# Performance work log

Hardware: AMD Instinct MI355X
Metric: run time of the kernel (lower is better)

The kernel has to match this reference:

```python
import jax, jax.numpy as jnp
import numpy as np

N = 50000   # nodes
E = 600000  # edges (avg degree 12)
D = 128     # embedding_dim == hidden_features
L = 4       # depth


def setup_inputs() -> dict:
    key = jax.random.key(0)
    k0, k1, k2, k3 = jax.random.split(key, 4)
    scale = 1.0 / np.sqrt(D)
    node_embedding = jax.random.normal(k0, (N, D), jnp.float32)
    edge_index = jax.random.randint(k1, (2, E), 0, N, dtype=jnp.int32)
    Ws_rel = jax.random.normal(k2, (L, D, D), jnp.float32) * scale
    bs_rel = jnp.zeros((L, D), jnp.float32)
    Ws_root = jax.random.normal(k3, (L, D, D), jnp.float32) * scale
    return {
        'node_embedding': node_embedding,
        'edge_index': edge_index,
        'Ws_rel': Ws_rel,
        'bs_rel': bs_rel,
        'Ws_root': Ws_root,
    }


def reference(node_embedding, edge_index, Ws_rel, bs_rel, Ws_root):
    # PyG GraphConv (aggr='mean'), flow source_to_target:
    #   out_i = lin_rel(mean_{j in N(i)} x_j) + lin_root(x_i)
    # followed by ELU (dropout probs are 0 -> identity).
    n = node_embedding.shape[0]
    src, dst = edge_index[0], edge_index[1]
    ones = jnp.ones((edge_index.shape[1],), node_embedding.dtype)
    deg = jax.ops.segment_sum(ones, dst, num_segments=n)
    inv_deg = (1.0 / jnp.maximum(deg, 1.0))[:, None]  # [n, 1]
    X = node_embedding
    for l in range(Ws_rel.shape[0]):
        agg = jax.ops.segment_sum(X[src], dst, num_segments=n) * inv_deg  # [n, D]
        out = agg @ Ws_rel[l] + bs_rel[l] + X @ Ws_root[l]
        X = jax.nn.elu(out)
    return X
```

## Files before the change

kernel.cpp:

```cpp
#include <hip/hip_runtime.h>

#define D 128
#define LDR 264
#define SLOTS 64
#define EPB 2048

typedef short bf16x8 __attribute__((ext_vector_type(8)));
typedef float f32x4 __attribute__((ext_vector_type(4)));

__device__ __forceinline__ unsigned short f2bf(float f) {
  unsigned int u = __float_as_uint(f);
  unsigned int r = (u + 0x7fff + ((u >> 16) & 1)) >> 16;
  return (unsigned short)r;
}
__device__ __forceinline__ unsigned int pack2bf(float lo, float hi) {
  return (unsigned int)f2bf(lo) | ((unsigned int)f2bf(hi) << 16);
}

__global__ __launch_bounds__(256) void k_build(
    const int* __restrict__ src, const int* __restrict__ dst, int E, int N,
    int* __restrict__ cursor, unsigned short* __restrict__ csr64,
    const float* __restrict__ X0, unsigned short* __restrict__ Xb, int total4,
    const float* __restrict__ Wrel, const float* __restrict__ Wroot,
    unsigned short* __restrict__ Wp, int wtot,
    int fb, int cb) {
  int b = blockIdx.x;
  if (b < fb) {
    int p = b & 7;
    int chunk = b >> 3;
    int lo = (int)((long long)p * N / 8);
    int hi = (int)((long long)(p + 1) * N / 8);
    int base = chunk * EPB + threadIdx.x;
#pragma unroll
    for (int it = 0; it < EPB / 256; ++it, base += 256) {
      if (base < E) {
        int d = dst[base];
        if (d >= lo && d < hi) {
          int ps = atomicAdd(&cursor[d], 1);
          if (ps < SLOTS) csr64[d * SLOTS + ps] = (unsigned short)src[base];
        }
      }
    }
    return;
  }
  b -= fb;
  if (b < cb) {
    int i = b * 256 + threadIdx.x;
    if (i < total4) {
      float4 v = ((const float4*)X0)[i];
      ushort4 o;
      o.x = f2bf(v.x); o.y = f2bf(v.y); o.z = f2bf(v.z); o.w = f2bf(v.w);
      ((ushort4*)Xb)[i] = o;
    }
    return;
  }
  b -= cb;
  {
    int gid = b * 256 + threadIdx.x;
    if (gid >= wtot) return;
    int lane = gid & 63;
    int t = gid >> 6;
    int ctg = t & 7; t >>= 3;
    int ks = t & 7; t >>= 3;
    int l = t;
    const float* Wr = Wrel + (size_t)l * D * D;
    const float* Wo = Wroot + (size_t)l * D * D;
    int colc = ctg * 16 + (lane & 15);
    int krow0 = ks * 32 + (lane >> 4) * 8;
    unsigned short tmp[8];
#pragma unroll
    for (int j = 0; j < 8; ++j) {
      int kr = krow0 + j;
      float w = (kr < D) ? Wr[(size_t)kr * D + colc] : Wo[(size_t)(kr - D) * D + colc];
      tmp[j] = f2bf(w);
    }
    unsigned short* dstp = Wp + ((size_t)gid) * 8;
#pragma unroll
    for (int j = 0; j < 8; ++j) dstp[j] = tmp[j];
  }
}


#define ACC8(v) \
    acc[0] += __uint_as_float((v).x << 16); acc[1] += __uint_as_float((v).x & 0xffff0000u); \
    acc[2] += __uint_as_float((v).y << 16); acc[3] += __uint_as_float((v).y & 0xffff0000u); \
    acc[4] += __uint_as_float((v).z << 16); acc[5] += __uint_as_float((v).z & 0xffff0000u); \
    acc[6] += __uint_as_float((v).w << 16); acc[7] += __uint_as_float((v).w & 0xffff0000u);

__global__ __launch_bounds__(256) void k_aggregate(const unsigned short* __restrict__ X,
    const int* __restrict__ cursor, const unsigned short* __restrict__ csr64,
    unsigned short* __restrict__ agg, int N) {
  int wave = (int)((blockIdx.x * blockDim.x + threadIdx.x) >> 6);
  int lane = threadIdx.x & 63;
  if (wave >= N) return;
  int grp = lane >> 4;
  int l16 = lane & 15;
  int deg = cursor[wave];
  int n = min(deg, SLOTS);
  int eid = (int)csr64[wave * SLOTS + lane];

  float acc[8];
#pragma unroll
  for (int k = 0; k < 8; ++k) acc[k] = 0.f;

  int j4 = 0;
  for (; j4 + 12 <= n; j4 += 12) {
    int s0 = __shfl(eid, j4 + grp);
    int s1 = __shfl(eid, j4 + 4 + grp);
    int s2 = __shfl(eid, j4 + 8 + grp);
    uint4 v0 = *(const uint4*)(X + (size_t)s0 * D + l16 * 8);
    uint4 v1 = *(const uint4*)(X + (size_t)s1 * D + l16 * 8);
    uint4 v2 = *(const uint4*)(X + (size_t)s2 * D + l16 * 8);
    ACC8(v0) ACC8(v1) ACC8(v2)
  }
  if (j4 + 8 <= n) {
    int s0 = __shfl(eid, j4 + grp);
    int s1 = __shfl(eid, j4 + 4 + grp);
    uint4 v0 = *(const uint4*)(X + (size_t)s0 * D + l16 * 8);
    uint4 v1 = *(const uint4*)(X + (size_t)s1 * D + l16 * 8);
    ACC8(v0) ACC8(v1)
    j4 += 8;
  }
  for (; j4 < n; j4 += 4) {
    int jj = j4 + grp;
    int s = __shfl(eid, jj);
    if (jj < n) {
      uint4 v = *(const uint4*)(X + (size_t)s * D + l16 * 8);
      ACC8(v)
    }
  }

#pragma unroll
  for (int k = 0; k < 8; ++k) {
    acc[k] += __shfl_xor(acc[k], 16);
    acc[k] += __shfl_xor(acc[k], 32);
  }

  if (grp == 0) {
    float inv = 1.0f / fmaxf((float)deg, 1.0f);
    uint4 o;
    o.x = pack2bf(acc[0] * inv, acc[1] * inv);
    o.y = pack2bf(acc[2] * inv, acc[3] * inv);
    o.z = pack2bf(acc[4] * inv, acc[5] * inv);
    o.w = pack2bf(acc[6] * inv, acc[7] * inv);
    *(uint4*)(agg + (size_t)wave * D + l16 * 8) = o;
  }
}

__global__ __launch_bounds__(256, 4) void k_layer(const unsigned short* __restrict__ agg,
    const unsigned short* __restrict__ Xin, const unsigned short* __restrict__ Wp_l,
    const float* __restrict__ bias, unsigned short* __restrict__ Xnext,
    float* __restrict__ out_f32, int last, int N) {
  __shared__ __align__(16) unsigned short sRow[64 * LDR];
  int tid = threadIdx.x;
  int r0 = blockIdx.x * 64;

  for (int i = tid; i < 64 * 32; i += 256) {
    int r = i >> 5, ch = i & 31;
    int row = r0 + r;
    uint4 v = make_uint4(0, 0, 0, 0);
    if (row < N) {
      const unsigned short* srcp = (ch < 16)
          ? (agg + (size_t)row * D + ch * 8)
          : (Xin + (size_t)row * D + (ch - 16) * 8);
      v = *(const uint4*)srcp;
    }
    *(uint4*)(&sRow[r * LDR + ch * 8]) = v;
  }
  __syncthreads();

  int wave = tid >> 6, lane = tid & 63;
  int m = lane & 15, q = lane >> 4;
  int ct0 = wave * 2;

  f32x4 acc[4][2];
#pragma unroll
  for (int g = 0; g < 4; ++g)
#pragma unroll
    for (int c = 0; c < 2; ++c) acc[g][c] = (f32x4){0.f, 0.f, 0.f, 0.f};

  const unsigned short* arow = &sRow[m * LDR + q * 8];
#pragma unroll
  for (int ks = 0; ks < 8; ++ks) {
    bf16x8 b0 = *(const bf16x8*)(Wp_l + ((size_t)((ks * 8 + ct0 + 0) * 64 + lane)) * 8);
    bf16x8 b1 = *(const bf16x8*)(Wp_l + ((size_t)((ks * 8 + ct0 + 1) * 64 + lane)) * 8);
    bf16x8 a0 = *(const bf16x8*)(arow + ks * 32);
    bf16x8 a1 = *(const bf16x8*)(arow + 16 * LDR + ks * 32);
    bf16x8 a2 = *(const bf16x8*)(arow + 32 * LDR + ks * 32);
    bf16x8 a3 = *(const bf16x8*)(arow + 48 * LDR + ks * 32);
    acc[0][0] = __builtin_amdgcn_mfma_f32_16x16x32_bf16(a0, b0, acc[0][0], 0, 0, 0);
    acc[0][1] = __builtin_amdgcn_mfma_f32_16x16x32_bf16(a0, b1, acc[0][1], 0, 0, 0);
    acc[1][0] = __builtin_amdgcn_mfma_f32_16x16x32_bf16(a1, b0, acc[1][0], 0, 0, 0);
    acc[1][1] = __builtin_amdgcn_mfma_f32_16x16x32_bf16(a1, b1, acc[1][1], 0, 0, 0);
    acc[2][0] = __builtin_amdgcn_mfma_f32_16x16x32_bf16(a2, b0, acc[2][0], 0, 0, 0);
    acc[2][1] = __builtin_amdgcn_mfma_f32_16x16x32_bf16(a2, b1, acc[2][1], 0, 0, 0);
    acc[3][0] = __builtin_amdgcn_mfma_f32_16x16x32_bf16(a3, b0, acc[3][0], 0, 0, 0);
    acc[3][1] = __builtin_amdgcn_mfma_f32_16x16x32_bf16(a3, b1, acc[3][1], 0, 0, 0);
  }

#pragma unroll
  for (int g = 0; g < 4; ++g) {
#pragma unroll
    for (int c = 0; c < 2; ++c) {
      int col = (ct0 + c) * 16 + m;
      float bv = bias[col];
      int rbase = r0 + g * 16 + q * 4;
#pragma unroll
      for (int j = 0; j < 4; ++j) {
        int row = rbase + j;
        float v = acc[g][c][j] + bv;
        float e = __expf(fminf(v, 0.f)) - 1.f;
        v = v > 0.f ? v : e;
        if (last) {
          if (row < N) out_f32[(size_t)row * D + col] = v;
        } else {
          unsigned int h = (unsigned int)f2bf(v);
          unsigned int nb = (unsigned int)__shfl_xor((int)h, 1);
          if (!(m & 1) && row < N)
            *(unsigned int*)(Xnext + (size_t)row * D + col) = h | (nb << 16);
        }
      }
    }
  }
}


extern "C" void kernel_launch(void* const* d_in, const int* in_sizes, int n_in,
                              void* d_out, int out_size, void* d_ws, size_t ws_size,
                              hipStream_t stream) {
  const float* X0    = (const float*)d_in[0];
  const int*   eidx  = (const int*)d_in[1];
  const float* Wrel  = (const float*)d_in[2];
  const float* brel  = (const float*)d_in[3];
  const float* Wroot = (const float*)d_in[4];
  float* out = (float*)d_out;

  const int N = in_sizes[0] / D;
  const int E = in_sizes[1] / 2;
  const int L = in_sizes[3] / D;
  const int* src = eidx;
  const int* dst = eidx + E;

  char* ws = (char*)d_ws;
  size_t off = 0;
  auto carve = [&](size_t bytes) -> void* {
    void* p = ws + off;
    off = (off + bytes + 255) & ~(size_t)255;
    return p;
  };
  unsigned short* Xb0  = (unsigned short*)carve((size_t)N * D * sizeof(unsigned short));
  unsigned short* Xb1  = (unsigned short*)carve((size_t)N * D * sizeof(unsigned short));
  unsigned short* aggb = (unsigned short*)carve((size_t)N * D * sizeof(unsigned short));
  unsigned short* Wp   = (unsigned short*)carve((size_t)L * 4096 * 8 * sizeof(unsigned short));
  int*            cursor = (int*)carve((size_t)N * sizeof(int));
  unsigned short* csr64  = (unsigned short*)carve((size_t)N * SLOTS * sizeof(unsigned short));
  (void)ws_size; (void)n_in; (void)out_size;

  hipMemsetAsync(cursor, 0, (size_t)N * sizeof(int), stream);

  const int chunks = (E + EPB - 1) / EPB;
  const int fb = chunks * 8;
  const int total4 = N * D / 4;
  const int cb = (total4 + 255) / 256;
  const int wtot = L * 4096;
  const int wb = (wtot + 255) / 256;
  k_build<<<fb + cb + wb, 256, 0, stream>>>(src, dst, E, N, cursor, csr64,
      X0, Xb0, total4, Wrel, Wroot, Wp, wtot, fb, cb);

  const int ab = (N + 3) / 4;
  const int lb = (N + 63) / 64;

  const unsigned short* Xcur = Xb0;
  for (int l = 0; l < L; ++l) {
    int last = (l == L - 1) ? 1 : 0;
    unsigned short* Xnext = (Xcur == Xb0) ? Xb1 : Xb0;
    k_aggregate<<<ab, 256, 0, stream>>>(Xcur, cursor, csr64, aggb, N);
    k_layer<<<lb, 256, 0, stream>>>(aggb, Xcur, Wp + (size_t)l * 4096 * 8,
        brel + (size_t)l * D, Xnext, out, last, N);
    Xcur = Xnext;
  }
}
```

Measured before the change: 258.9 us.

## Fuse neighbor aggregation into per-layer GEMM kernel via shared memory

Merges the gather-mean aggregation kernel into the layer MFMA kernel. Each wave aggregates 16 nodes serially and writes the bf16 means straight into the shared-memory A tile next to the root features, with a one-node-ahead prefetch of degree and edge ids. This removes the global round trip of the aggregated tensor and one launch per layer. In exchange, each wave handles 16 nodes sequentially with fewer waves in flight (782 blocks, 4 per CU), so the latency-bound gather may lose parallelism.

```diff
diff --git a/kernel.cpp b/kernel.cpp
--- a/kernel.cpp
+++ b/kernel.cpp
@@ -87,97 +87,104 @@
     acc[4] += __uint_as_float((v).z << 16); acc[5] += __uint_as_float((v).z & 0xffff0000u); \
     acc[6] += __uint_as_float((v).w << 16); acc[7] += __uint_as_float((v).w & 0xffff0000u);
 
-__global__ __launch_bounds__(256) void k_aggregate(const unsigned short* __restrict__ X,
+__global__ __launch_bounds__(256, 4) void k_layer_fused(
+    const unsigned short* __restrict__ Xin,
     const int* __restrict__ cursor, const unsigned short* __restrict__ csr64,
-    unsigned short* __restrict__ agg, int N) {
-  int wave = (int)((blockIdx.x * blockDim.x + threadIdx.x) >> 6);
-  int lane = threadIdx.x & 63;
-  if (wave >= N) return;
-  int grp = lane >> 4;
-  int l16 = lane & 15;
-  int deg = cursor[wave];
-  int n = min(deg, SLOTS);
-  int eid = (int)csr64[wave * SLOTS + lane];
-
-  float acc[8];
-#pragma unroll
-  for (int k = 0; k < 8; ++k) acc[k] = 0.f;
-
-  int j4 = 0;
-  for (; j4 + 12 <= n; j4 += 12) {
-    int s0 = __shfl(eid, j4 + grp);
-    int s1 = __shfl(eid, j4 + 4 + grp);
-    int s2 = __shfl(eid, j4 + 8 + grp);
-    uint4 v0 = *(const uint4*)(X + (size_t)s0 * D + l16 * 8);
-    uint4 v1 = *(const uint4*)(X + (size_t)s1 * D + l16 * 8);
-    uint4 v2 = *(const uint4*)(X + (size_t)s2 * D + l16 * 8);
-    ACC8(v0) ACC8(v1) ACC8(v2)
-  }
-  if (j4 + 8 <= n) {
-    int s0 = __shfl(eid, j4 + grp);
-    int s1 = __shfl(eid, j4 + 4 + grp);
-    uint4 v0 = *(const uint4*)(X + (size_t)s0 * D + l16 * 8);
-    uint4 v1 = *(const uint4*)(X + (size_t)s1 * D + l16 * 8);
-    ACC8(v0) ACC8(v1)
-    j4 += 8;
-  }
-  for (; j4 < n; j4 += 4) {
-    int jj = j4 + grp;
-    int s = __shfl(eid, jj);
-    if (jj < n) {
-      uint4 v = *(const uint4*)(X + (size_t)s * D + l16 * 8);
-      ACC8(v)
-    }
-  }
-
-#pragma unroll
-  for (int k = 0; k < 8; ++k) {
-    acc[k] += __shfl_xor(acc[k], 16);
-    acc[k] += __shfl_xor(acc[k], 32);
-  }
-
-  if (grp == 0) {
-    float inv = 1.0f / fmaxf((float)deg, 1.0f);
-    uint4 o;
-    o.x = pack2bf(acc[0] * inv, acc[1] * inv);
-    o.y = pack2bf(acc[2] * inv, acc[3] * inv);
-    o.z = pack2bf(acc[4] * inv, acc[5] * inv);
-    o.w = pack2bf(acc[6] * inv, acc[7] * inv);
-    *(uint4*)(agg + (size_t)wave * D + l16 * 8) = o;
-  }
-}
-
-__global__ __launch_bounds__(256, 4) void k_layer(const unsigned short* __restrict__ agg,
-    const unsigned short* __restrict__ Xin, const unsigned short* __restrict__ Wp_l,
-    const float* __restrict__ bias, unsigned short* __restrict__ Xnext,
-    float* __restrict__ out_f32, int last, int N) {
+    const unsigned short* __restrict__ Wp_l, const float* __restrict__ bias,
+    unsigned short* __restrict__ Xnext, float* __restrict__ out_f32,
+    int last, int N) {
   __shared__ __align__(16) unsigned short sRow[64 * LDR];
   int tid = threadIdx.x;
   int r0 = blockIdx.x * 64;
-
-  for (int i = tid; i < 64 * 32; i += 256) {
-    int r = i >> 5, ch = i & 31;
+  int wave = tid >> 6, lane = tid & 63;
+  int grp = lane >> 4;
+  int l16 = lane & 15;
+
+  for (int i = tid; i < 64 * 16; i += 256) {
+    int r = i >> 4, c = i & 15;
     int row = r0 + r;
-    uint4 v = make_uint4(0, 0, 0, 0);
-    if (row < N) {
-      const unsigned short* srcp = (ch < 16)
-          ? (agg + (size_t)row * D + ch * 8)
-          : (Xin + (size_t)row * D + (ch - 16) * 8);
-      v = *(const uint4*)srcp;
-    }
-    *(uint4*)(&sRow[r * LDR + ch * 8]) = v;
+    uint4 v = make_uint4(0u, 0u, 0u, 0u);
+    if (row < N) v = *(const uint4*)(Xin + (size_t)row * D + c * 8);
+    *(uint4*)(&sRow[r * LDR + (16 + c) * 8]) = v;
+  }
+
+  int node0 = r0 + wave * 16;
+  int deg_n = 0, eid_n = 0;
+  if (node0 < N) {
+    deg_n = cursor[node0];
+    eid_n = (int)csr64[(size_t)node0 * SLOTS + lane];
+  }
+  for (int k = 0; k < 16; ++k) {
+    int curnode = node0 + k;
+    int deg = deg_n;
+    int eid = eid_n;
+    int nxt = curnode + 1;
+    if (k < 15 && nxt < N) {
+      deg_n = cursor[nxt];
+      eid_n = (int)csr64[(size_t)nxt * SLOTS + lane];
+    } else {
+      deg_n = 0; eid_n = 0;
+    }
+
+    float acc[8];
+#pragma unroll
+    for (int t = 0; t < 8; ++t) acc[t] = 0.f;
+
+    if (curnode < N) {
+      int n = min(deg, SLOTS);
+      int j4 = 0;
+      for (; j4 + 12 <= n; j4 += 12) {
+        int s0 = __shfl(eid, j4 + grp);
+        int s1 = __shfl(eid, j4 + 4 + grp);
+        int s2 = __shfl(eid, j4 + 8 + grp);
+        uint4 v0 = *(const uint4*)(Xin + (size_t)s0 * D + l16 * 8);
+        uint4 v1 = *(const uint4*)(Xin + (size_t)s1 * D + l16 * 8);
+        uint4 v2 = *(const uint4*)(Xin + (size_t)s2 * D + l16 * 8);
+        ACC8(v0) ACC8(v1) ACC8(v2)
+      }
+      if (j4 + 8 <= n) {
+        int s0 = __shfl(eid, j4 + grp);
+        int s1 = __shfl(eid, j4 + 4 + grp);
+        uint4 v0 = *(const uint4*)(Xin + (size_t)s0 * D + l16 * 8);
+        uint4 v1 = *(const uint4*)(Xin + (size_t)s1 * D + l16 * 8);
+        ACC8(v0) ACC8(v1)
+        j4 += 8;
+      }
+      for (; j4 < n; j4 += 4) {
+        int jj = j4 + grp;
+        int s = __shfl(eid, jj);
+        if (jj < n) {
+          uint4 v = *(const uint4*)(Xin + (size_t)s * D + l16 * 8);
+          ACC8(v)
+        }
+      }
+#pragma unroll
+      for (int t = 0; t < 8; ++t) {
+        acc[t] += __shfl_xor(acc[t], 16);
+        acc[t] += __shfl_xor(acc[t], 32);
+      }
+    }
+
+    if (grp == 0) {
+      float inv = 1.0f / fmaxf((float)deg, 1.0f);
+      uint4 o;
+      o.x = pack2bf(acc[0] * inv, acc[1] * inv);
+      o.y = pack2bf(acc[2] * inv, acc[3] * inv);
+      o.z = pack2bf(acc[4] * inv, acc[5] * inv);
+      o.w = pack2bf(acc[6] * inv, acc[7] * inv);
+      *(uint4*)(&sRow[(wave * 16 + k) * LDR + l16 * 8]) = o;
+    }
   }
   __syncthreads();
 
-  int wave = tid >> 6, lane = tid & 63;
-  int m = lane & 15, q = lane >> 4;
+  int m = l16, q = grp;
   int ct0 = wave * 2;
 
-  f32x4 acc[4][2];
+  f32x4 cacc[4][2];
 #pragma unroll
   for (int g = 0; g < 4; ++g)
 #pragma unroll
-    for (int c = 0; c < 2; ++c) acc[g][c] = (f32x4){0.f, 0.f, 0.f, 0.f};
+    for (int c = 0; c < 2; ++c) cacc[g][c] = (f32x4){0.f, 0.f, 0.f, 0.f};
 
   const unsigned short* arow = &sRow[m * LDR + q * 8];
 #pragma unroll
@@ -188,14 +195,14 @@
     bf16x8 a1 = *(const bf16x8*)(arow + 16 * LDR + ks * 32);
     bf16x8 a2 = *(const bf16x8*)(arow + 32 * LDR + ks * 32);
     bf16x8 a3 = *(const bf16x8*)(arow + 48 * LDR + ks * 32);
-    acc[0][0] = __builtin_amdgcn_mfma_f32_16x16x32_bf16(a0, b0, acc[0][0], 0, 0, 0);
-    acc[0][1] = __builtin_amdgcn_mfma_f32_16x16x32_bf16(a0, b1, acc[0][1], 0, 0, 0);
-    acc[1][0] = __builtin_amdgcn_mfma_f32_16x16x32_bf16(a1, b0, acc[1][0], 0, 0, 0);
-    acc[1][1] = __builtin_amdgcn_mfma_f32_16x16x32_bf16(a1, b1, acc[1][1], 0, 0, 0);
-    acc[2][0] = __builtin_amdgcn_mfma_f32_16x16x32_bf16(a2, b0, acc[2][0], 0, 0, 0);
-    acc[2][1] = __builtin_amdgcn_mfma_f32_16x16x32_bf16(a2, b1, acc[2][1], 0, 0, 0);
-    acc[3][0] = __builtin_amdgcn_mfma_f32_16x16x32_bf16(a3, b0, acc[3][0], 0, 0, 0);
-    acc[3][1] = __builtin_amdgcn_mfma_f32_16x16x32_bf16(a3, b1, acc[3][1], 0, 0, 0);
+    cacc[0][0] = __builtin_amdgcn_mfma_f32_16x16x32_bf16(a0, b0, cacc[0][0], 0, 0, 0);
+    cacc[0][1] = __builtin_amdgcn_mfma_f32_16x16x32_bf16(a0, b1, cacc[0][1], 0, 0, 0);
+    cacc[1][0] = __builtin_amdgcn_mfma_f32_16x16x32_bf16(a1, b0, cacc[1][0], 0, 0, 0);
+    cacc[1][1] = __builtin_amdgcn_mfma_f32_16x16x32_bf16(a1, b1, cacc[1][1], 0, 0, 0);
+    cacc[2][0] = __builtin_amdgcn_mfma_f32_16x16x32_bf16(a2, b0, cacc[2][0], 0, 0, 0);
+    cacc[2][1] = __builtin_amdgcn_mfma_f32_16x16x32_bf16(a2, b1, cacc[2][1], 0, 0, 0);
+    cacc[3][0] = __builtin_amdgcn_mfma_f32_16x16x32_bf16(a3, b0, cacc[3][0], 0, 0, 0);
+    cacc[3][1] = __builtin_amdgcn_mfma_f32_16x16x32_bf16(a3, b1, cacc[3][1], 0, 0, 0);
   }
 
 #pragma unroll
@@ -208,7 +215,7 @@
 #pragma unroll
       for (int j = 0; j < 4; ++j) {
         int row = rbase + j;
-        float v = acc[g][c][j] + bv;
+        float v = cacc[g][c][j] + bv;
         float e = __expf(fminf(v, 0.f)) - 1.f;
         v = v > 0.f ? v : e;
         if (last) {
@@ -250,7 +257,6 @@
   };
   unsigned short* Xb0  = (unsigned short*)carve((size_t)N * D * sizeof(unsigned short));
   unsigned short* Xb1  = (unsigned short*)carve((size_t)N * D * sizeof(unsigned short));
-  unsigned short* aggb = (unsigned short*)carve((size_t)N * D * sizeof(unsigned short));
   unsigned short* Wp   = (unsigned short*)carve((size_t)L * 4096 * 8 * sizeof(unsigned short));
   int*            cursor = (int*)carve((size_t)N * sizeof(int));
   unsigned short* csr64  = (unsigned short*)carve((size_t)N * SLOTS * sizeof(unsigned short));
@@ -267,16 +273,14 @@
   k_build<<<fb + cb + wb, 256, 0, stream>>>(src, dst, E, N, cursor, csr64,
       X0, Xb0, total4, Wrel, Wroot, Wp, wtot, fb, cb);
 
-  const int ab = (N + 3) / 4;
   const int lb = (N + 63) / 64;
 
   const unsigned short* Xcur = Xb0;
   for (int l = 0; l < L; ++l) {
     int last = (l == L - 1) ? 1 : 0;
     unsigned short* Xnext = (Xcur == Xb0) ? Xb1 : Xb0;
-    k_aggregate<<<ab, 256, 0, stream>>>(Xcur, cursor, csr64, aggb, N);
-    k_layer<<<lb, 256, 0, stream>>>(aggb, Xcur, Wp + (size_t)l * 4096 * 8,
-        brel + (size_t)l * D, Xnext, out, last, N);
+    k_layer_fused<<<lb, 256, 0, stream>>>(Xcur, cursor, csr64,
+        Wp + (size_t)l * 4096 * 8, brel + (size_t)l * D, Xnext, out, last, N);
     Xcur = Xnext;
   }
 }
```

Result: slower. 283.9 us (+9.7%).

## Slice neighbor gather by feature column blocks to improve L2 locality

Applied to the files above, without the earlier changes.

Replaces the per-node wave aggregation with a kernel in which each block handles one of eight 16-column feature slices for 16 nodes. Each lane reads 8-byte pieces from up to 16 neighbors in parallel, so blocks of one slice touch only a 3.2MB column stripe of X, meant to fit in cache. The aggregate output goes to a slice-major layout that the layer kernel reads back. The cost is more, smaller global loads per edge, repeated reads of cursor and csr for each slice, and lower occupancy for low-degree nodes, since only n of 16 edge slots per pass do useful work.

```diff
diff --git a/kernel.cpp b/kernel.cpp
--- a/kernel.cpp
+++ b/kernel.cpp
@@ -80,74 +80,55 @@
   }
 }
 
-
-#define ACC8(v) \
-    acc[0] += __uint_as_float((v).x << 16); acc[1] += __uint_as_float((v).x & 0xffff0000u); \
-    acc[2] += __uint_as_float((v).y << 16); acc[3] += __uint_as_float((v).y & 0xffff0000u); \
-    acc[4] += __uint_as_float((v).z << 16); acc[5] += __uint_as_float((v).z & 0xffff0000u); \
-    acc[6] += __uint_as_float((v).w << 16); acc[7] += __uint_as_float((v).w & 0xffff0000u);
-
-__global__ __launch_bounds__(256) void k_aggregate(const unsigned short* __restrict__ X,
+__global__ __launch_bounds__(256) void k_gather_sliced(
+    const unsigned short* __restrict__ Xin,
     const int* __restrict__ cursor, const unsigned short* __restrict__ csr64,
-    unsigned short* __restrict__ agg, int N) {
-  int wave = (int)((blockIdx.x * blockDim.x + threadIdx.x) >> 6);
-  int lane = threadIdx.x & 63;
-  if (wave >= N) return;
-  int grp = lane >> 4;
-  int l16 = lane & 15;
-  int deg = cursor[wave];
-  int n = min(deg, SLOTS);
-  int eid = (int)csr64[wave * SLOTS + lane];
-
-  float acc[8];
-#pragma unroll
-  for (int k = 0; k < 8; ++k) acc[k] = 0.f;
-
-  int j4 = 0;
-  for (; j4 + 12 <= n; j4 += 12) {
-    int s0 = __shfl(eid, j4 + grp);
-    int s1 = __shfl(eid, j4 + 4 + grp);
-    int s2 = __shfl(eid, j4 + 8 + grp);
-    uint4 v0 = *(const uint4*)(X + (size_t)s0 * D + l16 * 8);
-    uint4 v1 = *(const uint4*)(X + (size_t)s1 * D + l16 * 8);
-    uint4 v2 = *(const uint4*)(X + (size_t)s2 * D + l16 * 8);
-    ACC8(v0) ACC8(v1) ACC8(v2)
-  }
-  if (j4 + 8 <= n) {
-    int s0 = __shfl(eid, j4 + grp);
-    int s1 = __shfl(eid, j4 + 4 + grp);
-    uint4 v0 = *(const uint4*)(X + (size_t)s0 * D + l16 * 8);
-    uint4 v1 = *(const uint4*)(X + (size_t)s1 * D + l16 * 8);
-    ACC8(v0) ACC8(v1)
-    j4 += 8;
-  }
-  for (; j4 < n; j4 += 4) {
-    int jj = j4 + grp;
-    int s = __shfl(eid, jj);
-    if (jj < n) {
-      uint4 v = *(const uint4*)(X + (size_t)s * D + l16 * 8);
-      ACC8(v)
-    }
-  }
-
-#pragma unroll
-  for (int k = 0; k < 8; ++k) {
-    acc[k] += __shfl_xor(acc[k], 16);
-    acc[k] += __shfl_xor(acc[k], 32);
-  }
-
-  if (grp == 0) {
-    float inv = 1.0f / fmaxf((float)deg, 1.0f);
-    uint4 o;
-    o.x = pack2bf(acc[0] * inv, acc[1] * inv);
-    o.y = pack2bf(acc[2] * inv, acc[3] * inv);
-    o.z = pack2bf(acc[4] * inv, acc[5] * inv);
-    o.w = pack2bf(acc[6] * inv, acc[7] * inv);
-    *(uint4*)(agg + (size_t)wave * D + l16 * 8) = o;
-  }
-}
-
-__global__ __launch_bounds__(256, 4) void k_layer(const unsigned short* __restrict__ agg,
+    unsigned short* __restrict__ aggs, int N) {
+  int slice = blockIdx.x & 7;
+  int sec = blockIdx.x >> 3;
+  int wave = threadIdx.x >> 6, lane = threadIdx.x & 63;
+  int e4 = lane >> 2;
+  int piece = lane & 3;
+  const unsigned short* Xs = Xin + slice * 16 + piece * 4;
+  int node0 = sec * 16 + wave * 4;
+#pragma unroll
+  for (int i = 0; i < 4; ++i) {
+    int node = node0 + i;
+    if (node >= N) return;
+    int deg = cursor[node];
+    int n = min(deg, SLOTS);
+    float a0 = 0.f, a1 = 0.f, a2 = 0.f, a3 = 0.f;
+    int nm1 = n - 1;
+    for (int r = 0; r * 16 < n; ++r) {
+      int j = r * 16 + e4;
+      int j2 = min(j, nm1);
+      int eid = (int)csr64[(size_t)node * SLOTS + j2];
+      uint2 v = *(const uint2*)(Xs + (size_t)eid * D);
+      if (j < n) {
+        a0 += __uint_as_float(v.x << 16);
+        a1 += __uint_as_float(v.x & 0xffff0000u);
+        a2 += __uint_as_float(v.y << 16);
+        a3 += __uint_as_float(v.y & 0xffff0000u);
+      }
+    }
+#pragma unroll
+    for (int mk = 4; mk <= 32; mk <<= 1) {
+      a0 += __shfl_xor(a0, mk);
+      a1 += __shfl_xor(a1, mk);
+      a2 += __shfl_xor(a2, mk);
+      a3 += __shfl_xor(a3, mk);
+    }
+    if (lane < 4) {
+      float inv = 1.0f / fmaxf((float)deg, 1.0f);
+      uint2 o;
+      o.x = pack2bf(a0 * inv, a1 * inv);
+      o.y = pack2bf(a2 * inv, a3 * inv);
+      *(uint2*)(aggs + ((size_t)slice * N + node) * 16 + piece * 4) = o;
+    }
+  }
+}
+
+__global__ __launch_bounds__(256, 4) void k_layer2(const unsigned short* __restrict__ aggs,
     const unsigned short* __restrict__ Xin, const unsigned short* __restrict__ Wp_l,
     const float* __restrict__ bias, unsigned short* __restrict__ Xnext,
     float* __restrict__ out_f32, int last, int N) {
@@ -161,7 +142,7 @@
     uint4 v = make_uint4(0, 0, 0, 0);
     if (row < N) {
       const unsigned short* srcp = (ch < 16)
-          ? (agg + (size_t)row * D + ch * 8)
+          ? (aggs + ((size_t)(ch >> 1) * N + row) * 16 + (ch & 1) * 8)
           : (Xin + (size_t)row * D + (ch - 16) * 8);
       v = *(const uint4*)srcp;
     }
@@ -250,10 +231,10 @@
   };
   unsigned short* Xb0  = (unsigned short*)carve((size_t)N * D * sizeof(unsigned short));
   unsigned short* Xb1  = (unsigned short*)carve((size_t)N * D * sizeof(unsigned short));
-  unsigned short* aggb = (unsigned short*)carve((size_t)N * D * sizeof(unsigned short));
   unsigned short* Wp   = (unsigned short*)carve((size_t)L * 4096 * 8 * sizeof(unsigned short));
   int*            cursor = (int*)carve((size_t)N * sizeof(int));
   unsigned short* csr64  = (unsigned short*)carve((size_t)N * SLOTS * sizeof(unsigned short));
+  unsigned short* aggs   = (unsigned short*)carve((size_t)8 * N * 16 * sizeof(unsigned short));
   (void)ws_size; (void)n_in; (void)out_size;
 
   hipMemsetAsync(cursor, 0, (size_t)N * sizeof(int), stream);
@@ -267,15 +248,15 @@
   k_build<<<fb + cb + wb, 256, 0, stream>>>(src, dst, E, N, cursor, csr64,
       X0, Xb0, total4, Wrel, Wroot, Wp, wtot, fb, cb);
 
-  const int ab = (N + 3) / 4;
+  const int gb = ((N + 15) / 16) * 8;
   const int lb = (N + 63) / 64;
 
   const unsigned short* Xcur = Xb0;
   for (int l = 0; l < L; ++l) {
     int last = (l == L - 1) ? 1 : 0;
     unsigned short* Xnext = (Xcur == Xb0) ? Xb1 : Xb0;
-    k_aggregate<<<ab, 256, 0, stream>>>(Xcur, cursor, csr64, aggb, N);
-    k_layer<<<lb, 256, 0, stream>>>(aggb, Xcur, Wp + (size_t)l * 4096 * 8,
+    k_gather_sliced<<<gb, 256, 0, stream>>>(Xcur, cursor, csr64, aggs, N);
+    k_layer2<<<lb, 256, 0, stream>>>(aggs, Xcur, Wp + (size_t)l * 4096 * 8,
         brel + (size_t)l * D, Xnext, out, last, N);
     Xcur = Xnext;
   }
```

Result: slower. 529.0 us (+104.3%).
